# Optimization experiments

Measured on AMD Instinct MI355X. Metric: run time of the kernel, lower is better.

The kernel has to match this reference:

```python
import math
import jax, jax.numpy as jnp
import numpy as np

DIM = 768
TARGET_DIM = 1024  # next power of two >= DIM


def _hadamard_matrix(n: int) -> np.ndarray:
    # Sylvester construction, normalized by 1/sqrt(n)
    H = np.array([[1.0]], dtype=np.float32)
    while H.shape[0] < n:
        H = np.block([[H, H], [H, -H]])
    return H / math.sqrt(n)


_H = jnp.asarray(_hadamard_matrix(TARGET_DIM))  # [1024, 1024]


def setup_inputs() -> dict:
    key = jax.random.key(0)
    x = jax.random.normal(key, (16, 768, 56, 56), dtype=jnp.float32)
    return {"x": x}


def reference(x):
    B, C, Hs, Ws = x.shape  # C == DIM
    # [B, C, H, W] -> [B, H, W, C] -> [B*H*W, C]
    xr = jnp.transpose(x, (0, 2, 3, 1)).reshape(-1, DIM)
    # pad channel dim up to TARGET_DIM
    xp = jnp.pad(xr, ((0, 0), (0, TARGET_DIM - DIM)))
    y = xp @ _H.astype(x.dtype)           # [B*H*W, 1024]
    y = y[:, :DIM]                        # slice back to dim
    y = y.reshape(B, Hs, Ws, C)
    return jnp.transpose(y, (0, 3, 1, 2))  # [B, C, H, W]
```

## Files before the change

### kernel.cpp

```cpp
#include <hip/hip_runtime.h>


#define NSPAT 3136
#define TS    32
#define NBPB  98
#define STQ   33
#define STI   793

#define FWHT_STAGE1(arr, D)                                  \
    _Pragma("unroll")                                        \
    for (int _b = 0; _b < 32; _b += 2 * (D)) {               \
        _Pragma("unroll")                                    \
        for (int _k = 0; _k < (D); ++_k) {                   \
            float _t = arr[_b + _k];                         \
            arr[_b + _k]       = _t + arr[_b + _k + (D)];    \
            arr[_b + _k + (D)] = _t - arr[_b + _k + (D)];    \
        }                                                    \
    }

__global__ __launch_bounds__(768, 6)
void hadamard_c768_kernel(const float* __restrict__ x, float* __restrict__ y) {
    __shared__ float lds[24 * STI];

    const int t   = threadIdx.x;
    const int bid = blockIdx.x;
    const int b   = bid / NBPB;
    const int s0  = (bid % NBPB) * TS;
    const int base = b * 768 * NSPAT + s0;

    const int g  = t >> 5;
    const int ln = t & 31;

    const float* __restrict__ xb = x + base;
    float*       __restrict__ yb = y + base;

    float a[32];
    const unsigned off0 = (unsigned)ln + (unsigned)(32 * g) * NSPAT;
    #pragma unroll
    for (int j = 0; j < 16; ++j)
        a[j] = xb[off0 + (unsigned)(j * NSPAT)];
    __builtin_amdgcn_sched_barrier(0);
    #pragma unroll
    for (int j = 16; j < 32; ++j)
        a[j] = xb[off0 + (unsigned)(j * NSPAT)];

    FWHT_STAGE1(a, 16)
    FWHT_STAGE1(a, 8)
    FWHT_STAGE1(a, 4)
    FWHT_STAGE1(a, 2)
    FWHT_STAGE1(a, 1)

    float* pw = lds + g * STI + ln;
    #pragma unroll
    for (int q = 0; q < 24; ++q)
        pw[q * STQ] = a[q];
    __syncthreads();

    float w[32];
    {
        const float* pr = lds + g * STQ + ln;
        #pragma unroll
        for (int i = 0; i < 24; ++i)
            w[i] = pr[i * STI];
    }
    __syncthreads();

    #pragma unroll
    for (int q = 0; q < 8; ++q)
        pw[q * STQ] = a[24 + q];
    __syncthreads();

    {
        #pragma unroll
        for (int i = 0; i < 8; ++i) {
            float tt  = w[i];
            w[i]      = tt + w[i + 16];
            w[i + 16] = tt - w[i + 16];
        }
        #pragma unroll
        for (int i = 8; i < 16; ++i)
            w[i + 16] = w[i];

        FWHT_STAGE1(w, 8)
        FWHT_STAGE1(w, 4)
        FWHT_STAGE1(w, 2)
        FWHT_STAGE1(w, 1)

        const unsigned oo = (unsigned)ln + (unsigned)g * NSPAT;
        #pragma unroll
        for (int pp = 0; pp < 24; ++pp)
            __builtin_nontemporal_store(w[pp] * 0.03125f,
                                        yb + oo + (unsigned)(pp * 32 * NSPAT));
    }

    {
        const int q8    = g & 7;
        const int pbase = (g >> 3) * 8;
        const float* pr = lds + q8 * STQ + ln;

        #pragma unroll
        for (int i = 0; i < 24; ++i)
            w[i] = pr[i * STI];

        #pragma unroll
        for (int i = 0; i < 8; ++i) {
            float tt  = w[i];
            w[i]      = tt + w[i + 16];
            w[i + 16] = tt - w[i + 16];
        }
        #pragma unroll
        for (int i = 8; i < 16; ++i)
            w[i + 16] = w[i];

        FWHT_STAGE1(w, 8)
        FWHT_STAGE1(w, 4)
        FWHT_STAGE1(w, 2)
        FWHT_STAGE1(w, 1)

        const unsigned o1 = (unsigned)ln
                          + (unsigned)(24 + q8) * NSPAT
                          + (unsigned)(pbase * 32) * NSPAT;
        #pragma unroll
        for (int pp = 0; pp < 8; ++pp)
            __builtin_nontemporal_store(w[pbase + pp] * 0.03125f,
                                        yb + o1 + (unsigned)(pp * 32 * NSPAT));
    }
}

extern "C" void kernel_launch(void* const* d_in, const int* in_sizes, int n_in,
                              void* d_out, int out_size, void* d_ws, size_t ws_size,
                              hipStream_t stream) {
    const float* x = (const float*)d_in[0];
    float*       y = (float*)d_out;
    const int nblocks = 16 * NBPB;
    hadamard_c768_kernel<<<dim3(nblocks), dim3(768), 0, stream>>>(x, y);
}
```

Baseline: 298.7 us.

## Use 1024-thread blocks so each wave handles one output quad in one pass

Blocks grow from 768 to 1024 threads so the 32 transposed quad groups are handled by 32 wavefronts in a single LDS exchange. The two-phase write/read with an extra barrier and second transform pass is removed, and the LDS stride grows to hold all 32 quads. Only 24 wavefronts load input, so 8 sit idle during the load phase. The larger LDS footprint and tighter launch bounds may limit occupancy or register allocation.

```diff
diff --git a/kernel.cpp b/kernel.cpp
--- a/kernel.cpp
+++ b/kernel.cpp
@@ -5,7 +5,7 @@
 #define TS    32
 #define NBPB  98
 #define STQ   33
-#define STI   793
+#define STI   1057
 
 #define FWHT_STAGE1(arr, D)                                  \
     _Pragma("unroll")                                        \
@@ -18,7 +18,7 @@
         }                                                    \
     }
 
-__global__ __launch_bounds__(768, 6)
+__global__ __launch_bounds__(1024, 4)
 void hadamard_c768_kernel(const float* __restrict__ x, float* __restrict__ y) {
     __shared__ float lds[24 * STI];
 
@@ -34,43 +34,33 @@
     const float* __restrict__ xb = x + base;
     float*       __restrict__ yb = y + base;
 
-    float a[32];
-    const unsigned off0 = (unsigned)ln + (unsigned)(32 * g) * NSPAT;
-    #pragma unroll
-    for (int j = 0; j < 16; ++j)
-        a[j] = xb[off0 + (unsigned)(j * NSPAT)];
-    __builtin_amdgcn_sched_barrier(0);
-    #pragma unroll
-    for (int j = 16; j < 32; ++j)
-        a[j] = xb[off0 + (unsigned)(j * NSPAT)];
+    if (g < 24) {
+        float a[32];
+        const unsigned off0 = (unsigned)ln + (unsigned)(32 * g) * NSPAT;
+        #pragma unroll
+        for (int j = 0; j < 32; ++j)
+            a[j] = xb[off0 + (unsigned)(j * NSPAT)];
 
-    FWHT_STAGE1(a, 16)
-    FWHT_STAGE1(a, 8)
-    FWHT_STAGE1(a, 4)
-    FWHT_STAGE1(a, 2)
-    FWHT_STAGE1(a, 1)
+        FWHT_STAGE1(a, 16)
+        FWHT_STAGE1(a, 8)
+        FWHT_STAGE1(a, 4)
+        FWHT_STAGE1(a, 2)
+        FWHT_STAGE1(a, 1)
 
-    float* pw = lds + g * STI + ln;
-    #pragma unroll
-    for (int q = 0; q < 24; ++q)
-        pw[q * STQ] = a[q];
+        float* pw = lds + g * STI + ln;
+        #pragma unroll
+        for (int q = 0; q < 32; ++q)
+            pw[q * STQ] = a[q];
+    }
     __syncthreads();
 
-    float w[32];
     {
+        float w[32];
         const float* pr = lds + g * STQ + ln;
         #pragma unroll
         for (int i = 0; i < 24; ++i)
             w[i] = pr[i * STI];
-    }
-    __syncthreads();
 
-    #pragma unroll
-    for (int q = 0; q < 8; ++q)
-        pw[q * STQ] = a[24 + q];
-    __syncthreads();
-
-    {
         #pragma unroll
         for (int i = 0; i < 8; ++i) {
             float tt  = w[i];
@@ -92,39 +82,6 @@
             __builtin_nontemporal_store(w[pp] * 0.03125f,
                                         yb + oo + (unsigned)(pp * 32 * NSPAT));
     }
-
-    {
-        const int q8    = g & 7;
-        const int pbase = (g >> 3) * 8;
-        const float* pr = lds + q8 * STQ + ln;
-
-        #pragma unroll
-        for (int i = 0; i < 24; ++i)
-            w[i] = pr[i * STI];
-
-        #pragma unroll
-        for (int i = 0; i < 8; ++i) {
-            float tt  = w[i];
-            w[i]      = tt + w[i + 16];
-            w[i + 16] = tt - w[i + 16];
-        }
-        #pragma unroll
-        for (int i = 8; i < 16; ++i)
-            w[i + 16] = w[i];
-
-        FWHT_STAGE1(w, 8)
-        FWHT_STAGE1(w, 4)
-        FWHT_STAGE1(w, 2)
-        FWHT_STAGE1(w, 1)
-
-        const unsigned o1 = (unsigned)ln
-                          + (unsigned)(24 + q8) * NSPAT
-                          + (unsigned)(pbase * 32) * NSPAT;
-        #pragma unroll
-        for (int pp = 0; pp < 8; ++pp)
-            __builtin_nontemporal_store(w[pbase + pp] * 0.03125f,
-                                        yb + o1 + (unsigned)(pp * 32 * NSPAT));
-    }
 }
 
 extern "C" void kernel_launch(void* const* d_in, const int* in_sizes, int n_in,
@@ -133,5 +90,5 @@
     const float* x = (const float*)d_in[0];
     float*       y = (float*)d_out;
     const int nblocks = 16 * NBPB;
-    hadamard_c768_kernel<<<dim3(nblocks), dim3(768), 0, stream>>>(x, y);
+    hadamard_c768_kernel<<<dim3(nblocks), dim3(1024), 0, stream>>>(x, y);
 }
```

Result: faster. 265.6 us (-11.1%).
